# Kernel tuning notes

Measured on AMD Instinct MI355X. Metric: run time of the kernel, lower is better.

## Reference

```python
import jax, jax.numpy as jnp
import numpy as np

N, E, G = 100000, 1600000, 512
D_IN, D_H, D_OUT = 128, 128, 1
EPS = 1e-5


def _gcn_conv(x, W, b, src, dst, n):
    # PyG GCNConv: h = x @ W, add self-loops, symmetric-normalized sum aggregation, bias after.
    h = x @ W
    loop = jnp.arange(n)
    s = jnp.concatenate([src, loop])
    d = jnp.concatenate([dst, loop])
    deg = jax.ops.segment_sum(jnp.ones(s.shape[0], dtype=h.dtype), d, num_segments=n)
    dinv = jnp.where(deg > 0, jax.lax.rsqrt(deg), 0.0)
    norm = dinv[s] * dinv[d]  # [E+N]
    out = jax.ops.segment_sum(h[s] * norm[:, None], d, num_segments=n)
    return out + b


def _bn(x, g, b, m, v):
    # eval-mode BatchNorm1d
    return (x - m) * jax.lax.rsqrt(v + EPS) * g + b


def setup_inputs() -> dict:
    key = jax.random.key(0)
    ks = jax.random.split(key, 24)
    x = jax.random.normal(ks[0], (N, D_IN), dtype=jnp.float32)
    edge_index = jax.random.randint(ks[1], (2, E), 0, N, dtype=jnp.int64)
    batch = (jnp.arange(N, dtype=jnp.int64) * G) // N  # sorted, all graphs non-empty
    inp = {"x": x, "edge_index": edge_index, "batch": batch}
    dims = [(D_IN, D_H), (D_H, D_H), (D_H, D_H)]
    for i, (din, dout) in enumerate(dims):
        sc = 1.0 / np.sqrt(din)
        inp[f"W{i}"] = jax.random.normal(ks[2 + 4 * i], (din, dout), dtype=jnp.float32) * sc
        inp[f"cb{i}"] = jnp.zeros((dout,), dtype=jnp.float32)
        inp[f"g{i}"] = jnp.ones((dout,), dtype=jnp.float32)
        inp[f"bt{i}"] = jnp.zeros((dout,), dtype=jnp.float32)
        inp[f"m{i}"] = jax.random.normal(ks[3 + 4 * i], (dout,), dtype=jnp.float32) * 0.1
        inp[f"v{i}"] = jax.random.uniform(ks[4 + 4 * i], (dout,), dtype=jnp.float32, minval=0.5, maxval=1.5)
    inp["L1w"] = jax.random.normal(ks[15], (2 * D_H, D_H), dtype=jnp.float32) / np.sqrt(2 * D_H)
    inp["L1b"] = jnp.zeros((D_H,), dtype=jnp.float32)
    inp["L2w"] = jax.random.normal(ks[16], (D_H, D_H // 2), dtype=jnp.float32) / np.sqrt(D_H)
    inp["L2b"] = jnp.zeros((D_H // 2,), dtype=jnp.float32)
    inp["L3w"] = jax.random.normal(ks[17], (D_H // 2, D_OUT), dtype=jnp.float32) / np.sqrt(D_H // 2)
    inp["L3b"] = jnp.zeros((D_OUT,), dtype=jnp.float32)
    return inp


def reference(x, edge_index, batch,
              W0, cb0, g0, bt0, m0, v0,
              W1, cb1, g1, bt1, m1, v1,
              W2, cb2, g2, bt2, m2, v2,
              L1w, L1b, L2w, L2b, L3w, L3b):
    src, dst = edge_index[0], edge_index[1]
    Ws = [W0, W1, W2]
    cbs = [cb0, cb1, cb2]
    bns = [(g0, bt0, m0, v0), (g1, bt1, m1, v1), (g2, bt2, m2, v2)]
    for i in range(3):
        x_prev = x
        x = _gcn_conv(x, Ws[i], cbs[i], src, dst, N)
        x = jax.nn.relu(_bn(x, *bns[i]))
        # dropout is identity in eval mode
        if i > 0:
            x = x + x_prev  # residual (shapes match for i > 0)
    ones = jnp.ones((N,), dtype=x.dtype)
    cnt = jax.ops.segment_sum(ones, batch, num_segments=G)[:, None]
    x_mean = jax.ops.segment_sum(x, batch, num_segments=G) / cnt
    x_max = jax.ops.segment_max(x, batch, num_segments=G)
    h = jnp.concatenate([x_mean, x_max], axis=1)  # [G, 2*D_H]
    h = jax.nn.relu(h @ L1w + L1b)
    h = jax.nn.relu(h @ L2w + L2b)
    return h @ L3w + L3b  # [G, 1]
```

## Files before the change

### kernel.cpp

```cpp
#include <hip/hip_runtime.h>
#include <math.h>

#define DH 128
#define EPSB 1e-5f
#define MAXB 832
#define BCAP 3072

typedef __attribute__((ext_vector_type(8))) short short8;
typedef __attribute__((ext_vector_type(4))) float f32x4;

static __device__ __forceinline__ unsigned short f2bf(float f) {
    unsigned u = __float_as_uint(f);
    u += 0x7fffu + ((u >> 16) & 1u);
    return (unsigned short)(u >> 16);
}
static __device__ __forceinline__ float bf2f(unsigned short h) {
    return __uint_as_float(((unsigned)h) << 16);
}


__global__ void k_bounds(const int* __restrict__ batch, int* __restrict__ starts, int N, int G) {
    int i = blockIdx.x * blockDim.x + threadIdx.x;
    if (i < N) {
        int b = batch[i];
        if (i == 0) { starts[0] = 0; starts[G] = N; }
        else if (batch[i - 1] != b) starts[b] = i;
    }
}


__launch_bounds__(256)
__global__ void k_bucketA(const int* __restrict__ src, const int* __restrict__ dst,
                          int* __restrict__ gcur, int* __restrict__ bbuf,
                          int E, int NB, int chunk)
{
    __shared__ int cnt[MAXB];
    __shared__ int base[MAXB];
    const int t = threadIdx.x;
    for (int i = t; i < NB; i += 256) cnt[i] = 0;
    __syncthreads();
    const int e0 = blockIdx.x * chunk;
    const int e1 = min(E, e0 + chunk);
    for (int e = e0 + t; e < e1; e += 256)
        atomicAdd(&cnt[dst[e] >> 7], 1);
    __syncthreads();
    for (int i = t; i < NB; i += 256) {
        int c = cnt[i];
        base[i] = (c > 0) ? atomicAdd(&gcur[i], c) : 0;
        cnt[i] = 0;
    }
    __syncthreads();
    for (int e = e0 + t; e < e1; e += 256) {
        int d = dst[e];
        int b = d >> 7;
        int o = base[b] + atomicAdd(&cnt[b], 1);
        if (o < BCAP) bbuf[(size_t)b * BCAP + o] = (src[e] << 7) | (d & 127);
    }
}

__launch_bounds__(1024)
__global__ void k_bgscan(const int* __restrict__ gcur, int* __restrict__ bbase,
                         int* __restrict__ rowptr, int NB, int N, int E)
{
    __shared__ int s[1024];
    int t = threadIdx.x;
    int v = (t < NB) ? min(gcur[t], BCAP) : 0;
    s[t] = v;
    __syncthreads();
    for (int off = 1; off < 1024; off <<= 1) {
        int u = (t >= off) ? s[t - off] : 0;
        __syncthreads();
        s[t] += u;
        __syncthreads();
    }
    if (t < NB) bbase[t] = s[t] - v;
    if (t == 0) rowptr[N] = E;
}

__launch_bounds__(256)
__global__ void k_bfinal(const int* __restrict__ gcur, const int* __restrict__ bbase,
                         const int* __restrict__ bbuf, int* __restrict__ rowptr,
                         float* __restrict__ dinv, int* __restrict__ csr_src, int N)
{
    __shared__ int ebuf[BCAP];
    __shared__ int dcnt[128];
    __shared__ int sp[128];
    const int b = blockIdx.x, t = threadIdx.x;
    const int c = min(gcur[b], BCAP);
    const int base = bbase[b];
    const int* p = bbuf + (size_t)b * BCAP;
    for (int i = t; i < c; i += 256) ebuf[i] = p[i];
    if (t < 128) dcnt[t] = 0;
    __syncthreads();
    for (int i = t; i < c; i += 256) atomicAdd(&dcnt[ebuf[i] & 127], 1);
    __syncthreads();
    if (t < 128) sp[t] = dcnt[t];
    __syncthreads();
    for (int off = 1; off < 128; off <<= 1) {
        int u = (t < 128 && t >= off) ? sp[t - off] : 0;
        __syncthreads();
        if (t < 128) sp[t] += u;
        __syncthreads();
    }
    if (t < 128) {
        sp[t] -= dcnt[t];
        int d = b * 128 + t;
        if (d < N) {
            rowptr[d] = base + sp[t];
            dinv[d] = rsqrtf((float)(dcnt[t] + 1));
        }
        dcnt[t] = 0;
    }
    __syncthreads();
    for (int i = t; i < c; i += 256) {
        int e = ebuf[i];
        int dl = e & 127;
        int o = atomicAdd(&dcnt[dl], 1);
        csr_src[base + sp[dl] + o] = e >> 7;
    }
}


__global__ void k_wfrag(const float* __restrict__ W0, const float* __restrict__ W1,
                        const float* __restrict__ W2, unsigned short* __restrict__ Wf0) {
    int l = blockIdx.x >> 6;
    int f = blockIdx.x & 63;
    int lane = threadIdx.x;
    const float* W = (l == 0) ? W0 : (l == 1) ? W1 : W2;
    unsigned short* Wf = Wf0 + (size_t)l * 32768;
    int nt = f & 3, s = (f >> 2) & 3, p = (f >> 4) & 1, nh = f >> 5;
    int n = nh * 64 + nt * 16 + (lane & 15);
    int kbase = s * 32 + (lane >> 4) * 8;
    unsigned short o[8];
#pragma unroll
    for (int j = 0; j < 8; ++j) {
        float w = W[(size_t)(kbase + j) * DH + n];
        unsigned short h = f2bf(w);
        o[j] = p ? f2bf(w - bf2f(h)) : h;
    }
    unsigned short* d = Wf + (size_t)f * 512 + lane * 8;
    *(ushort4*)d       = make_ushort4(o[0], o[1], o[2], o[3]);
    *(ushort4*)(d + 4) = make_ushort4(o[4], o[5], o[6], o[7]);
}


__launch_bounds__(256)
__global__ void k_gemm_mfma(const float* __restrict__ X,
                            const unsigned short* __restrict__ Wf,
                            const float* __restrict__ dinv,
                            unsigned short* __restrict__ hs, int N)
{
    __shared__ float As[64 * DH];

    const int tid  = threadIdx.x;
    const int lane = tid & 63, wave = tid >> 6;
    const int mh = wave >> 1, nh = wave & 1;
    const int rowBase = blockIdx.x * 64;
    const int r15 = lane & 15, quad = lane >> 4;

    {
        const float4* gp = (const float4*)(X + (size_t)rowBase * DH);
        float4* sp = (float4*)As;
#pragma unroll
        for (int it = 0; it < 8; ++it) {
            int idx = it * 256 + tid;
            int grow = idx >> 5;
            float4 v = make_float4(0.f, 0.f, 0.f, 0.f);
            if (rowBase + grow < N) v = gp[idx];
            sp[idx] = v;
        }
    }
    __syncthreads();

    f32x4 acc[2][4];
#pragma unroll
    for (int mt = 0; mt < 2; ++mt)
#pragma unroll
        for (int nt = 0; nt < 4; ++nt)
            acc[mt][nt] = (f32x4){0.f, 0.f, 0.f, 0.f};

#pragma unroll
    for (int s = 0; s < 4; ++s) {
        short8 wfh[4], wfl[4];
#pragma unroll
        for (int nt = 0; nt < 4; ++nt) {
            wfh[nt] = *(const short8*)(Wf + ((((nh * 2 + 0) * 4 + s) * 4 + nt) * 512) + lane * 8);
            wfl[nt] = *(const short8*)(Wf + ((((nh * 2 + 1) * 4 + s) * 4 + nt) * 512) + lane * 8);
        }
#pragma unroll
        for (int mt = 0; mt < 2; ++mt) {
            const float* ap = As + (mh * 32 + mt * 16 + r15) * DH + s * 32 + quad * 8;
            short8 ah, al;
#pragma unroll
            for (int j = 0; j < 8; ++j) {
                float v = ap[j];
                unsigned short h = f2bf(v);
                ah[j] = (short)h;
                al[j] = (short)f2bf(v - bf2f(h));
            }
#pragma unroll
            for (int nt = 0; nt < 4; ++nt) {
                acc[mt][nt] = __builtin_amdgcn_mfma_f32_16x16x32_bf16(ah, wfh[nt], acc[mt][nt], 0, 0, 0);
                acc[mt][nt] = __builtin_amdgcn_mfma_f32_16x16x32_bf16(ah, wfl[nt], acc[mt][nt], 0, 0, 0);
                acc[mt][nt] = __builtin_amdgcn_mfma_f32_16x16x32_bf16(al, wfh[nt], acc[mt][nt], 0, 0, 0);
            }
        }
    }

#pragma unroll
    for (int mt = 0; mt < 2; ++mt) {
        int rl = mh * 32 + mt * 16 + quad * 4;
#pragma unroll
        for (int reg = 0; reg < 4; ++reg) {
            int row = rowBase + rl + reg;
            if (row < N) {
                float sc = dinv[row];
#pragma unroll
                for (int nt = 0; nt < 4; ++nt)
                    hs[(size_t)row * DH + nh * 64 + nt * 16 + r15] = f2bf(acc[mt][nt][reg] * sc);
            }
        }
    }
}


__launch_bounds__(256)
__global__ void k_gather(const unsigned short* __restrict__ hs, const int* __restrict__ rowptr,
                         const int* __restrict__ csr_src, const float* __restrict__ dinv,
                         const float* __restrict__ cb, const float* __restrict__ bm,
                         const float* __restrict__ bv, const float* __restrict__ bg,
                         const float* __restrict__ bb, const float* __restrict__ prev,
                         float* __restrict__ xout, int N)
{
    const int node = (blockIdx.x * blockDim.x + threadIdx.x) >> 5;
    const int lh = threadIdx.x & 31;
    if (node >= N) return;
    const int f = lh * 4;
    const int e0 = rowptr[node], e1 = rowptr[node + 1];

    ushort4 su = *(const ushort4*)(hs + (size_t)node * DH + f);
    float a0 = bf2f(su.x), a1 = bf2f(su.y), a2 = bf2f(su.z), a3 = bf2f(su.w);

    for (int base = e0; base < e1; base += 32) {
        int cnt = e1 - base; if (cnt > 32) cnt = 32;
        int idx = (lh < cnt) ? csr_src[base + lh] : 0;
        int i = 0;
        for (; i + 4 <= cnt; i += 4) {
            int s0 = __shfl(idx, i,     32), s1 = __shfl(idx, i + 1, 32);
            int s2 = __shfl(idx, i + 2, 32), s3 = __shfl(idx, i + 3, 32);
            ushort4 v0 = *(const ushort4*)(hs + (size_t)s0 * DH + f);
            ushort4 v1 = *(const ushort4*)(hs + (size_t)s1 * DH + f);
            ushort4 v2 = *(const ushort4*)(hs + (size_t)s2 * DH + f);
            ushort4 v3 = *(const ushort4*)(hs + (size_t)s3 * DH + f);
            a0 += (bf2f(v0.x) + bf2f(v1.x)) + (bf2f(v2.x) + bf2f(v3.x));
            a1 += (bf2f(v0.y) + bf2f(v1.y)) + (bf2f(v2.y) + bf2f(v3.y));
            a2 += (bf2f(v0.z) + bf2f(v1.z)) + (bf2f(v2.z) + bf2f(v3.z));
            a3 += (bf2f(v0.w) + bf2f(v1.w)) + (bf2f(v2.w) + bf2f(v3.w));
        }
        for (; i < cnt; ++i) {
            int s = __shfl(idx, i, 32);
            ushort4 v = *(const ushort4*)(hs + (size_t)s * DH + f);
            a0 += bf2f(v.x); a1 += bf2f(v.y); a2 += bf2f(v.z); a3 += bf2f(v.w);
        }
    }

    const float sc = dinv[node];
    const float4 vcb = *(const float4*)(cb + f);
    const float4 vbm = *(const float4*)(bm + f);
    const float4 vbv = *(const float4*)(bv + f);
    const float4 vbg = *(const float4*)(bg + f);
    const float4 vbb = *(const float4*)(bb + f);
    float o0 = (a0 * sc + vcb.x - vbm.x) * rsqrtf(vbv.x + EPSB) * vbg.x + vbb.x;
    float o1 = (a1 * sc + vcb.y - vbm.y) * rsqrtf(vbv.y + EPSB) * vbg.y + vbb.y;
    float o2 = (a2 * sc + vcb.z - vbm.z) * rsqrtf(vbv.z + EPSB) * vbg.z + vbb.z;
    float o3 = (a3 * sc + vcb.w - vbm.w) * rsqrtf(vbv.w + EPSB) * vbg.w + vbb.w;
    o0 = fmaxf(o0, 0.f); o1 = fmaxf(o1, 0.f); o2 = fmaxf(o2, 0.f); o3 = fmaxf(o3, 0.f);
    if (prev) {
        const float4 p = *(const float4*)(prev + (size_t)node * DH + f);
        o0 += p.x; o1 += p.y; o2 += p.z; o3 += p.w;
    }
    *(float4*)(xout + (size_t)node * DH + f) = make_float4(o0, o1, o2, o3);
}


__launch_bounds__(128)
__global__ void k_pool_mlp(const float* __restrict__ x, const int* __restrict__ starts,
                           const float* __restrict__ L1w, const float* __restrict__ L1b,
                           const float* __restrict__ L2w, const float* __restrict__ L2b,
                           const float* __restrict__ L3w, const float* __restrict__ L3b,
                           float* __restrict__ out)
{
    int g = blockIdx.x, t = threadIdx.x;
    int s0 = starts[g], s1 = starts[g + 1];
    float su0 = 0.f, su1 = 0.f, su2 = 0.f, su3 = 0.f;
    float m0 = -INFINITY, m1 = -INFINITY, m2 = -INFINITY, m3 = -INFINITY;
    int i = s0;
    for (; i + 4 <= s1; i += 4) {
        float v0 = x[(size_t)i * DH + t];
        float v1 = x[(size_t)(i + 1) * DH + t];
        float v2 = x[(size_t)(i + 2) * DH + t];
        float v3 = x[(size_t)(i + 3) * DH + t];
        su0 += v0; su1 += v1; su2 += v2; su3 += v3;
        m0 = fmaxf(m0, v0); m1 = fmaxf(m1, v1);
        m2 = fmaxf(m2, v2); m3 = fmaxf(m3, v3);
    }
    for (; i < s1; ++i) {
        float v = x[(size_t)i * DH + t];
        su0 += v; m0 = fmaxf(m0, v);
    }
    float sum = (su0 + su1) + (su2 + su3);
    float mx = fmaxf(fmaxf(m0, m1), fmaxf(m2, m3));

    __shared__ float h[256];
    h[t] = sum / (float)(s1 - s0);
    h[128 + t] = mx;
    __syncthreads();

    float a = L1b[t];
    for (int k = 0; k < 256; ++k) a += h[k] * L1w[k * DH + t];
    __shared__ float h1[128];
    h1[t] = fmaxf(a, 0.f);
    __syncthreads();

    __shared__ float h2[64];
    if (t < 64) {
        float a2 = L2b[t];
        for (int k = 0; k < 128; ++k) a2 += h1[k] * L2w[k * 64 + t];
        h2[t] = fmaxf(a2, 0.f);
    }
    __syncthreads();

    if (t < 64) {
        float p = h2[t] * L3w[t];
#pragma unroll
        for (int off = 32; off > 0; off >>= 1) p += __shfl_down(p, off, 64);
        if (t == 0) out[g] = p + L3b[0];
    }
}


static inline char* align16(char* p) {
    return (char*)(((uintptr_t)p + 15) & ~(uintptr_t)15);
}

extern "C" void kernel_launch(void* const* d_in, const int* in_sizes, int n_in,
                              void* d_out, int out_size, void* d_ws, size_t ws_size,
                              hipStream_t stream)
{
    const float* x     = (const float*)d_in[0];
    const int*   ei    = (const int*)d_in[1];
    const int*   batch = (const int*)d_in[2];
    const int N = in_sizes[0] / DH;
    const int E = in_sizes[1] / 2;
    const int G = out_size;
    const int* src = ei;
    const int* dst = ei + E;

    const float* W[3]  = {(const float*)d_in[3],  (const float*)d_in[9],  (const float*)d_in[15]};
    const float* cb[3] = {(const float*)d_in[4],  (const float*)d_in[10], (const float*)d_in[16]};
    const float* bg[3] = {(const float*)d_in[5],  (const float*)d_in[11], (const float*)d_in[17]};
    const float* bt[3] = {(const float*)d_in[6],  (const float*)d_in[12], (const float*)d_in[18]};
    const float* bm[3] = {(const float*)d_in[7],  (const float*)d_in[13], (const float*)d_in[19]};
    const float* bv[3] = {(const float*)d_in[8],  (const float*)d_in[14], (const float*)d_in[20]};
    const float* L1w = (const float*)d_in[21]; const float* L1b = (const float*)d_in[22];
    const float* L2w = (const float*)d_in[23]; const float* L2b = (const float*)d_in[24];
    const float* L3w = (const float*)d_in[25]; const float* L3b = (const float*)d_in[26];

    char* wsp = (char*)d_ws;
    size_t big = (size_t)N * DH * sizeof(float);
    unsigned short* HS = (unsigned short*)wsp; wsp += (size_t)N * DH * sizeof(unsigned short);
    float* P1 = (float*)wsp;  wsp += big;
    float* P2 = (float*)wsp;  wsp += big;
    unsigned short* Wfrag = (unsigned short*)wsp; wsp += 3 * 65536;
    float* dinv   = (float*)wsp; wsp += (size_t)N * sizeof(float);
    int*   rowptr = (int*)wsp;   wsp = align16(wsp + (size_t)(N + 1) * sizeof(int));
    int*   csr_src= (int*)wsp;   wsp += (size_t)E * sizeof(int);
    int*   starts = (int*)wsp;   wsp = align16(wsp + (size_t)(G + 1) * sizeof(int));
    int*   gcur   = (int*)wsp;   wsp = align16(wsp + (size_t)MAXB * sizeof(int));
    int*   bbase  = (int*)wsp;   wsp = align16(wsp + (size_t)MAXB * sizeof(int));
    int*   bbuf   = (int*)wsp;   wsp += (size_t)MAXB * BCAP * sizeof(int);

    const int NB = (N + 127) >> 7;
    const int nblkA = 128;
    const int chunk = (E + nblkA - 1) / nblkA;

    hipMemsetAsync(gcur, 0, (size_t)NB * sizeof(int), stream);
    k_bucketA<<<nblkA, 256, 0, stream>>>(src, dst, gcur, bbuf, E, NB, chunk);
    k_bgscan <<<1, 1024, 0, stream>>>(gcur, bbase, rowptr, NB, N, E);
    k_bfinal <<<NB, 256, 0, stream>>>(gcur, bbase, bbuf, rowptr, dinv, csr_src, N);
    k_bounds <<<(N + 255) / 256, 256, 0, stream>>>(batch, starts, N, G);
    k_wfrag  <<<192, 64, 0, stream>>>(W[0], W[1], W[2], Wfrag);

    const float* Xs[3]    = {x, P1, P2};
    const float* prevb[3] = {nullptr, P1, P2};
    float* xoutb[3]       = {P1, P2, P1};

    int gemmGrid = (N + 63) / 64;
    int gathGrid = ((size_t)N * 32 + 255) / 256;

    for (int l = 0; l < 3; ++l) {
        k_gemm_mfma<<<gemmGrid, 256, 0, stream>>>(Xs[l], Wfrag + (size_t)l * 32768,
                                                  dinv, HS, N);
        k_gather<<<gathGrid, 256, 0, stream>>>(HS, rowptr, csr_src, dinv,
                                               cb[l], bm[l], bv[l], bg[l], bt[l],
                                               prevb[l], xoutb[l], N);
    }

    k_pool_mlp<<<G, 128, 0, stream>>>(xoutb[2], starts, L1w, L1b, L2w, L2b, L3w, L3b,
                                      (float*)d_out);
}
```

Before: 521.6 us.

## Store layer activations as split bf16 hi/lo planes and pad GEMM LDS

Layer outputs are now written by the gather kernel as two bf16 planes (hi and residual lo) instead of fp32. The later GEMMs then load pre-split operands straight into padded LDS, with no per-element conversion, and pooling reads the two planes. The change also pads the first GEMM's LDS stride to avoid bank conflicts, folds the batch-bounds kernel into the bucketing kernel, and packs four weight fragments per wfrag block. Memory traffic per activation stays the same (2×2 bytes versus 4), so the expected gain comes from dropping conversion work, fewer launches and fewer LDS conflicts. The hi+lo form carries slightly less precision than fp32.

```diff
diff --git a/kernel.cpp b/kernel.cpp
--- a/kernel.cpp
+++ b/kernel.cpp
@@ -19,24 +19,22 @@
 }
 
 
-__global__ void k_bounds(const int* __restrict__ batch, int* __restrict__ starts, int N, int G) {
-    int i = blockIdx.x * blockDim.x + threadIdx.x;
-    if (i < N) {
+__launch_bounds__(256)
+__global__ void k_bucketA(const int* __restrict__ src, const int* __restrict__ dst,
+                          int* __restrict__ gcur, int* __restrict__ bbuf,
+                          const int* __restrict__ batch, int* __restrict__ starts,
+                          int E, int NB, int chunk, int N, int G)
+{
+    __shared__ int cnt[MAXB];
+    __shared__ int base[MAXB];
+    const int t = threadIdx.x;
+
+    for (int i = blockIdx.x * 256 + t; i < N; i += gridDim.x * 256) {
         int b = batch[i];
         if (i == 0) { starts[0] = 0; starts[G] = N; }
         else if (batch[i - 1] != b) starts[b] = i;
     }
-}
-
-
-__launch_bounds__(256)
-__global__ void k_bucketA(const int* __restrict__ src, const int* __restrict__ dst,
-                          int* __restrict__ gcur, int* __restrict__ bbuf,
-                          int E, int NB, int chunk)
-{
-    __shared__ int cnt[MAXB];
-    __shared__ int base[MAXB];
-    const int t = threadIdx.x;
+
     for (int i = t; i < NB; i += 256) cnt[i] = 0;
     __syncthreads();
     const int e0 = blockIdx.x * chunk;
@@ -123,9 +121,10 @@
 
 __global__ void k_wfrag(const float* __restrict__ W0, const float* __restrict__ W1,
                         const float* __restrict__ W2, unsigned short* __restrict__ Wf0) {
-    int l = blockIdx.x >> 6;
-    int f = blockIdx.x & 63;
-    int lane = threadIdx.x;
+    int fid = blockIdx.x * 4 + (threadIdx.x >> 6);
+    int lane = threadIdx.x & 63;
+    int l = fid >> 6;
+    int f = fid & 63;
     const float* W = (l == 0) ? W0 : (l == 1) ? W1 : W2;
     unsigned short* Wf = Wf0 + (size_t)l * 32768;
     int nt = f & 3, s = (f >> 2) & 3, p = (f >> 4) & 1, nh = f >> 5;
@@ -144,13 +143,15 @@
 }
 
 
+#define LDA0 132
+
 __launch_bounds__(256)
-__global__ void k_gemm_mfma(const float* __restrict__ X,
-                            const unsigned short* __restrict__ Wf,
-                            const float* __restrict__ dinv,
-                            unsigned short* __restrict__ hs, int N)
-{
-    __shared__ float As[64 * DH];
+__global__ void k_gemm0(const float* __restrict__ X,
+                        const unsigned short* __restrict__ Wf,
+                        const float* __restrict__ dinv,
+                        unsigned short* __restrict__ hs, int N)
+{
+    __shared__ float As[64 * LDA0];
 
     const int tid  = threadIdx.x;
     const int lane = tid & 63, wave = tid >> 6;
@@ -160,14 +161,13 @@
 
     {
         const float4* gp = (const float4*)(X + (size_t)rowBase * DH);
-        float4* sp = (float4*)As;
 #pragma unroll
         for (int it = 0; it < 8; ++it) {
             int idx = it * 256 + tid;
-            int grow = idx >> 5;
+            int grow = idx >> 5, gcol = idx & 31;
             float4 v = make_float4(0.f, 0.f, 0.f, 0.f);
             if (rowBase + grow < N) v = gp[idx];
-            sp[idx] = v;
+            *(float4*)(As + grow * LDA0 + gcol * 4) = v;
         }
     }
     __syncthreads();
@@ -189,7 +189,7 @@
         }
 #pragma unroll
         for (int mt = 0; mt < 2; ++mt) {
-            const float* ap = As + (mh * 32 + mt * 16 + r15) * DH + s * 32 + quad * 8;
+            const float* ap = As + (mh * 32 + mt * 16 + r15) * LDA0 + s * 32 + quad * 8;
             short8 ah, al;
 #pragma unroll
             for (int j = 0; j < 8; ++j) {
@@ -224,13 +224,96 @@
 }
 
 
+#define LDAP 136
+
+__launch_bounds__(256)
+__global__ void k_gemm_pl(const unsigned short* __restrict__ Xh,
+                          const unsigned short* __restrict__ Xl,
+                          const unsigned short* __restrict__ Wf,
+                          const float* __restrict__ dinv,
+                          unsigned short* __restrict__ hs, int N)
+{
+    __shared__ unsigned short Ah[64 * LDAP];
+    __shared__ unsigned short Al[64 * LDAP];
+
+    const int tid  = threadIdx.x;
+    const int lane = tid & 63, wave = tid >> 6;
+    const int mh = wave >> 1, nh = wave & 1;
+    const int rowBase = blockIdx.x * 64;
+    const int r15 = lane & 15, quad = lane >> 4;
+
+    {
+        const uint4* gh = (const uint4*)(Xh + (size_t)rowBase * DH);
+        const uint4* gl = (const uint4*)(Xl + (size_t)rowBase * DH);
+#pragma unroll
+        for (int it = 0; it < 4; ++it) {
+            int idx = it * 256 + tid;
+            int grow = idx >> 4, gcol8 = (idx & 15) * 8;
+            uint4 vh = make_uint4(0, 0, 0, 0), vl = make_uint4(0, 0, 0, 0);
+            if (rowBase + grow < N) { vh = gh[idx]; vl = gl[idx]; }
+            *(uint4*)(Ah + grow * LDAP + gcol8) = vh;
+            *(uint4*)(Al + grow * LDAP + gcol8) = vl;
+        }
+    }
+    __syncthreads();
+
+    f32x4 acc[2][4];
+#pragma unroll
+    for (int mt = 0; mt < 2; ++mt)
+#pragma unroll
+        for (int nt = 0; nt < 4; ++nt)
+            acc[mt][nt] = (f32x4){0.f, 0.f, 0.f, 0.f};
+
+#pragma unroll
+    for (int s = 0; s < 4; ++s) {
+        short8 wfh[4], wfl[4];
+#pragma unroll
+        for (int nt = 0; nt < 4; ++nt) {
+            wfh[nt] = *(const short8*)(Wf + ((((nh * 2 + 0) * 4 + s) * 4 + nt) * 512) + lane * 8);
+            wfl[nt] = *(const short8*)(Wf + ((((nh * 2 + 1) * 4 + s) * 4 + nt) * 512) + lane * 8);
+        }
+#pragma unroll
+        for (int mt = 0; mt < 2; ++mt) {
+            int arow = mh * 32 + mt * 16 + r15;
+            short8 ah = *(const short8*)(Ah + arow * LDAP + s * 32 + quad * 8);
+            short8 al = *(const short8*)(Al + arow * LDAP + s * 32 + quad * 8);
+#pragma unroll
+            for (int nt = 0; nt < 4; ++nt) {
+                acc[mt][nt] = __builtin_amdgcn_mfma_f32_16x16x32_bf16(ah, wfh[nt], acc[mt][nt], 0, 0, 0);
+                acc[mt][nt] = __builtin_amdgcn_mfma_f32_16x16x32_bf16(ah, wfl[nt], acc[mt][nt], 0, 0, 0);
+                acc[mt][nt] = __builtin_amdgcn_mfma_f32_16x16x32_bf16(al, wfh[nt], acc[mt][nt], 0, 0, 0);
+            }
+        }
+    }
+
+#pragma unroll
+    for (int mt = 0; mt < 2; ++mt) {
+        int rl = mh * 32 + mt * 16 + quad * 4;
+#pragma unroll
+        for (int reg = 0; reg < 4; ++reg) {
+            int row = rowBase + rl + reg;
+            if (row < N) {
+                float sc = dinv[row];
+#pragma unroll
+                for (int nt = 0; nt < 4; ++nt)
+                    hs[(size_t)row * DH + nh * 64 + nt * 16 + r15] = f2bf(acc[mt][nt][reg] * sc);
+            }
+        }
+    }
+}
+
+
 __launch_bounds__(256)
 __global__ void k_gather(const unsigned short* __restrict__ hs, const int* __restrict__ rowptr,
                          const int* __restrict__ csr_src, const float* __restrict__ dinv,
                          const float* __restrict__ cb, const float* __restrict__ bm,
                          const float* __restrict__ bv, const float* __restrict__ bg,
-                         const float* __restrict__ bb, const float* __restrict__ prev,
-                         float* __restrict__ xout, int N)
+                         const float* __restrict__ bb,
+                         const unsigned short* __restrict__ ph,
+                         const unsigned short* __restrict__ pl,
+                         unsigned short* __restrict__ oh,
+                         unsigned short* __restrict__ ol,
+                         int N)
 {
     const int node = (blockIdx.x * blockDim.x + threadIdx.x) >> 5;
     const int lh = threadIdx.x & 31;
@@ -275,16 +358,26 @@
     float o2 = (a2 * sc + vcb.z - vbm.z) * rsqrtf(vbv.z + EPSB) * vbg.z + vbb.z;
     float o3 = (a3 * sc + vcb.w - vbm.w) * rsqrtf(vbv.w + EPSB) * vbg.w + vbb.w;
     o0 = fmaxf(o0, 0.f); o1 = fmaxf(o1, 0.f); o2 = fmaxf(o2, 0.f); o3 = fmaxf(o3, 0.f);
-    if (prev) {
-        const float4 p = *(const float4*)(prev + (size_t)node * DH + f);
-        o0 += p.x; o1 += p.y; o2 += p.z; o3 += p.w;
-    }
-    *(float4*)(xout + (size_t)node * DH + f) = make_float4(o0, o1, o2, o3);
+    if (ph) {
+        ushort4 hv = *(const ushort4*)(ph + (size_t)node * DH + f);
+        ushort4 lv = *(const ushort4*)(pl + (size_t)node * DH + f);
+        o0 += bf2f(hv.x) + bf2f(lv.x);
+        o1 += bf2f(hv.y) + bf2f(lv.y);
+        o2 += bf2f(hv.z) + bf2f(lv.z);
+        o3 += bf2f(hv.w) + bf2f(lv.w);
+    }
+    unsigned short h0 = f2bf(o0), h1 = f2bf(o1), h2 = f2bf(o2), h3 = f2bf(o3);
+    *(ushort4*)(oh + (size_t)node * DH + f) = make_ushort4(h0, h1, h2, h3);
+    *(ushort4*)(ol + (size_t)node * DH + f) =
+        make_ushort4(f2bf(o0 - bf2f(h0)), f2bf(o1 - bf2f(h1)),
+                     f2bf(o2 - bf2f(h2)), f2bf(o3 - bf2f(h3)));
 }
 
 
 __launch_bounds__(128)
-__global__ void k_pool_mlp(const float* __restrict__ x, const int* __restrict__ starts,
+__global__ void k_pool_mlp(const unsigned short* __restrict__ xh,
+                           const unsigned short* __restrict__ xl,
+                           const int* __restrict__ starts,
                            const float* __restrict__ L1w, const float* __restrict__ L1b,
                            const float* __restrict__ L2w, const float* __restrict__ L2b,
                            const float* __restrict__ L3w, const float* __restrict__ L3b,
@@ -292,28 +385,35 @@
 {
     int g = blockIdx.x, t = threadIdx.x;
     int s0 = starts[g], s1 = starts[g + 1];
-    float su0 = 0.f, su1 = 0.f, su2 = 0.f, su3 = 0.f;
-    float m0 = -INFINITY, m1 = -INFINITY, m2 = -INFINITY, m3 = -INFINITY;
-    int i = s0;
-    for (; i + 4 <= s1; i += 4) {
-        float v0 = x[(size_t)i * DH + t];
-        float v1 = x[(size_t)(i + 1) * DH + t];
-        float v2 = x[(size_t)(i + 2) * DH + t];
-        float v3 = x[(size_t)(i + 3) * DH + t];
-        su0 += v0; su1 += v1; su2 += v2; su3 += v3;
-        m0 = fmaxf(m0, v0); m1 = fmaxf(m1, v1);
-        m2 = fmaxf(m2, v2); m3 = fmaxf(m3, v3);
-    }
-    for (; i < s1; ++i) {
-        float v = x[(size_t)i * DH + t];
-        su0 += v; m0 = fmaxf(m0, v);
-    }
-    float sum = (su0 + su1) + (su2 + su3);
-    float mx = fmaxf(fmaxf(m0, m1), fmaxf(m2, m3));
+    const int half = t >> 6;
+    const int tc = t & 63;
+    const int fc = tc * 2;
+
+    float sA = 0.f, sB = 0.f;
+    float mA = -INFINITY, mB = -INFINITY;
+    for (int i = s0 + half; i < s1; i += 2) {
+        unsigned hv = *(const unsigned*)(xh + (size_t)i * DH + fc);
+        unsigned lv = *(const unsigned*)(xl + (size_t)i * DH + fc);
+        float vA = bf2f((unsigned short)hv) + bf2f((unsigned short)lv);
+        float vB = bf2f((unsigned short)(hv >> 16)) + bf2f((unsigned short)(lv >> 16));
+        sA += vA; sB += vB;
+        mA = fmaxf(mA, vA); mB = fmaxf(mB, vB);
+    }
+
+    __shared__ float ps[2][128];
+    __shared__ float pm[2][128];
+    ps[half][fc] = sA; ps[half][fc + 1] = sB;
+    pm[half][fc] = mA; pm[half][fc + 1] = mB;
+    __syncthreads();
 
     __shared__ float h[256];
-    h[t] = sum / (float)(s1 - s0);
-    h[128 + t] = mx;
+    if (half == 0) {
+        float inv = 1.f / (float)(s1 - s0);
+        h[fc]     = (ps[0][fc]     + ps[1][fc])     * inv;
+        h[fc + 1] = (ps[0][fc + 1] + ps[1][fc + 1]) * inv;
+        h[128 + fc]     = fmaxf(pm[0][fc],     pm[1][fc]);
+        h[128 + fc + 1] = fmaxf(pm[0][fc + 1], pm[1][fc + 1]);
+    }
     __syncthreads();
 
     float a = L1b[t];
@@ -367,10 +467,12 @@
     const float* L3w = (const float*)d_in[25]; const float* L3b = (const float*)d_in[26];
 
     char* wsp = (char*)d_ws;
-    size_t big = (size_t)N * DH * sizeof(float);
-    unsigned short* HS = (unsigned short*)wsp; wsp += (size_t)N * DH * sizeof(unsigned short);
-    float* P1 = (float*)wsp;  wsp += big;
-    float* P2 = (float*)wsp;  wsp += big;
+    size_t planeB = (size_t)N * DH * sizeof(unsigned short);
+    unsigned short* HS  = (unsigned short*)wsp; wsp += planeB;
+    unsigned short* AH  = (unsigned short*)wsp; wsp += planeB;
+    unsigned short* AL  = (unsigned short*)wsp; wsp += planeB;
+    unsigned short* BH  = (unsigned short*)wsp; wsp += planeB;
+    unsigned short* BL  = (unsigned short*)wsp; wsp += planeB;
     unsigned short* Wfrag = (unsigned short*)wsp; wsp += 3 * 65536;
     float* dinv   = (float*)wsp; wsp += (size_t)N * sizeof(float);
     int*   rowptr = (int*)wsp;   wsp = align16(wsp + (size_t)(N + 1) * sizeof(int));
@@ -385,27 +487,28 @@
     const int chunk = (E + nblkA - 1) / nblkA;
 
     hipMemsetAsync(gcur, 0, (size_t)NB * sizeof(int), stream);
-    k_bucketA<<<nblkA, 256, 0, stream>>>(src, dst, gcur, bbuf, E, NB, chunk);
+    k_bucketA<<<nblkA, 256, 0, stream>>>(src, dst, gcur, bbuf, batch, starts,
+                                         E, NB, chunk, N, G);
     k_bgscan <<<1, 1024, 0, stream>>>(gcur, bbase, rowptr, NB, N, E);
     k_bfinal <<<NB, 256, 0, stream>>>(gcur, bbase, bbuf, rowptr, dinv, csr_src, N);
-    k_bounds <<<(N + 255) / 256, 256, 0, stream>>>(batch, starts, N, G);
-    k_wfrag  <<<192, 64, 0, stream>>>(W[0], W[1], W[2], Wfrag);
-
-    const float* Xs[3]    = {x, P1, P2};
-    const float* prevb[3] = {nullptr, P1, P2};
-    float* xoutb[3]       = {P1, P2, P1};
+    k_wfrag  <<<48, 256, 0, stream>>>(W[0], W[1], W[2], Wfrag);
 
     int gemmGrid = (N + 63) / 64;
     int gathGrid = ((size_t)N * 32 + 255) / 256;
 
-    for (int l = 0; l < 3; ++l) {
-        k_gemm_mfma<<<gemmGrid, 256, 0, stream>>>(Xs[l], Wfrag + (size_t)l * 32768,
-                                                  dinv, HS, N);
-        k_gather<<<gathGrid, 256, 0, stream>>>(HS, rowptr, csr_src, dinv,
-                                               cb[l], bm[l], bv[l], bg[l], bt[l],
-                                               prevb[l], xoutb[l], N);
-    }
-
-    k_pool_mlp<<<G, 128, 0, stream>>>(xoutb[2], starts, L1w, L1b, L2w, L2b, L3w, L3b,
+    k_gemm0<<<gemmGrid, 256, 0, stream>>>(x, Wfrag, dinv, HS, N);
+    k_gather<<<gathGrid, 256, 0, stream>>>(HS, rowptr, csr_src, dinv,
+                                           cb[0], bm[0], bv[0], bg[0], bt[0],
+                                           nullptr, nullptr, AH, AL, N);
+    k_gemm_pl<<<gemmGrid, 256, 0, stream>>>(AH, AL, Wfrag + 32768, dinv, HS, N);
+    k_gather<<<gathGrid, 256, 0, stream>>>(HS, rowptr, csr_src, dinv,
+                                           cb[1], bm[1], bv[1], bg[1], bt[1],
+                                           AH, AL, BH, BL, N);
+    k_gemm_pl<<<gemmGrid, 256, 0, stream>>>(BH, BL, Wfrag + 65536, dinv, HS, N);
+    k_gather<<<gathGrid, 256, 0, stream>>>(HS, rowptr, csr_src, dinv,
+                                           cb[2], bm[2], bv[2], bg[2], bt[2],
+                                           BH, BL, AH, AL, N);
+
+    k_pool_mlp<<<G, 128, 0, stream>>>(AH, AL, starts, L1w, L1b, L2w, L2b, L3w, L3b,
                                       (float*)d_out);
 }
```

Result: no change. 530.1 us (+1.6%).
